# Kernel tuning notes

Measured on AMD Instinct MI355X. Metric: run time of the kernel, lower is better.

The kernel has to match this reference:

```python
import jax, jax.numpy as jnp
import numpy as np

B, T, D = 2, 4096, 768
H = 12
DK = D // H


def setup_inputs() -> dict:
    key = jax.random.key(0)
    k1, k2, k3 = jax.random.split(key, 3)
    x = jax.random.normal(k1, (B, T, D), dtype=jnp.float32)
    W_qkv = jax.random.normal(k2, (D, 3 * D), dtype=jnp.float32) * (1.0 / np.sqrt(D))
    b_qkv = jnp.zeros((3 * D,), dtype=jnp.float32)
    W_proj = jax.random.normal(k3, (D, D), dtype=jnp.float32) * (1.0 / np.sqrt(D))
    b_proj = jnp.zeros((D,), dtype=jnp.float32)
    return {"x": x, "W_qkv": W_qkv, "b_qkv": b_qkv, "W_proj": W_proj, "b_proj": b_proj}


def reference(x, W_qkv, b_qkv, W_proj, b_proj):
    b, t, c = x.shape
    qkv = x @ W_qkv + b_qkv                      # [B,T,3D]
    q, k, v = jnp.split(qkv, 3, axis=-1)
    q = q.reshape(b, t, H, DK)                   # [B,T,H,DK]
    k = k.reshape(b, t, H, DK)
    v = v.reshape(b, t, H, DK)
    scale = 1.0 / np.sqrt(DK)
    scores = jnp.einsum('bthd,bshd->bhts', q, k) * scale   # [B,H,T,T]
    causal = jnp.tril(jnp.ones((t, t), dtype=bool))
    scores = jnp.where(causal[None, None], scores, jnp.float32(-jnp.inf))
    probs = jax.nn.softmax(scores, axis=-1)      # dropout p=0.0 -> identity
    out = jnp.einsum('bhts,bshd->bthd', probs, v).reshape(b, t, c)
    return out @ W_proj + b_proj
```

## Files before the change

### kernel.cpp

```cpp
#include <hip/hip_runtime.h>
#include <hip/hip_bf16.h>
#include <cstdint>
#include <cstddef>


typedef __attribute__((ext_vector_type(8))) short bf16x8;
typedef __attribute__((ext_vector_type(4))) short bf16x4;
typedef __attribute__((ext_vector_type(4))) float f32x4;

#define MFMA16(a, b, c)   __builtin_amdgcn_mfma_f32_16x16x32_bf16((a), (b), (c), 0, 0, 0)
#define MFMA16K(a, b, c)  __builtin_amdgcn_mfma_f32_16x16x16bf16_1k((a), (b), (c), 0, 0, 0)

static constexpr int Bc = 2, Tc = 4096, Dc = 768, Hc = 12, DKc = 64;
static constexpr int BHc = Bc * Hc;
static constexpr int Mc = Bc * Tc;
static constexpr int Nqkv = 3 * Dc;
static constexpr int NQBLK = Tc / 128;
static constexpr unsigned int NITEMS = BHc * NQBLK;

__device__ __forceinline__ unsigned short f2bf(float f) {
    union { float f; unsigned int i; } c; c.f = f;
    unsigned int x = c.i;
    return (unsigned short)((x + 0x7fffu + ((x >> 16) & 1u)) >> 16);
}
__device__ __forceinline__ unsigned int pkbf(float a, float b) {
    __hip_bfloat162 h = __float22bfloat162_rn(make_float2(a, b));
    union { __hip_bfloat162 h; unsigned int u; } c; c.h = h;
    return c.u;
}
__device__ __forceinline__ void glds16(const unsigned short* g, unsigned short* l) {
    __builtin_amdgcn_global_load_lds(
        (const __attribute__((address_space(1))) unsigned int*)g,
        (__attribute__((address_space(3))) unsigned int*)l, 16, 0, 0);
}

__global__ __launch_bounds__(256)
void xconv_kernel(const float* __restrict__ X, unsigned short* __restrict__ Xb) {
    size_t i = ((size_t)blockIdx.x * 256 + threadIdx.x) * 8;
    float4 a = *(const float4*)(X + i);
    float4 b = *(const float4*)(X + i + 4);
    uint4 o;
    o.x = pkbf(a.x, a.y); o.y = pkbf(a.z, a.w);
    o.z = pkbf(b.x, b.y); o.w = pkbf(b.z, b.w);
    *(uint4*)(Xb + i) = o;
}

__global__ __launch_bounds__(256)
void wtrans_kernel(const float* __restrict__ W, unsigned short* __restrict__ WT,
                   int K, int N) {
    __shared__ __align__(16) unsigned short tile[64 * 72];
    const int k0 = blockIdx.x * 64;
    const int n0 = blockIdx.y * 64;
    const int tid = threadIdx.x;
#pragma unroll
    for (int it = 0; it < 4; ++it) {
        int s = tid + it * 256;
        int r = s >> 4, g = s & 15;
        float4 v = *(const float4*)(W + (size_t)(k0 + r) * N + n0 + g * 4);
        ushort4 u;
        u.x = f2bf(v.x); u.y = f2bf(v.y); u.z = f2bf(v.z); u.w = f2bf(v.w);
        *(ushort4*)(tile + r * 72 + g * 4) = u;
    }
    __syncthreads();
#pragma unroll
    for (int it = 0; it < 2; ++it) {
        int s = tid + it * 256;
        int n = s >> 3, g = s & 7;
        unsigned int p0 = (unsigned int)tile[(g * 8 + 0) * 72 + n] |
                          ((unsigned int)tile[(g * 8 + 1) * 72 + n] << 16);
        unsigned int p1 = (unsigned int)tile[(g * 8 + 2) * 72 + n] |
                          ((unsigned int)tile[(g * 8 + 3) * 72 + n] << 16);
        unsigned int p2 = (unsigned int)tile[(g * 8 + 4) * 72 + n] |
                          ((unsigned int)tile[(g * 8 + 5) * 72 + n] << 16);
        unsigned int p3 = (unsigned int)tile[(g * 8 + 6) * 72 + n] |
                          ((unsigned int)tile[(g * 8 + 7) * 72 + n] << 16);
        uint4 o; o.x = p0; o.y = p1; o.z = p2; o.w = p3;
        *(uint4*)(WT + (size_t)(n0 + n) * K + k0 + g * 8) = o;
    }
}

__global__ __launch_bounds__(256)
void qkv_gemm_kernel(const unsigned short* __restrict__ Xb,
                     const unsigned short* __restrict__ WT,
                     const float* __restrict__ bias,
                     unsigned short* __restrict__ Qb, unsigned short* __restrict__ Kb,
                     unsigned short* __restrict__ Vt) {
    __shared__ __align__(16) unsigned short As[128 * 64];
    __shared__ __align__(16) unsigned short Bs[128 * 64];
    const int tid = threadIdx.x;
    const int wave = tid >> 6, lane = tid & 63;
    const int quad = lane >> 4, l15 = lane & 15;
    const int wr = wave >> 1, wc = wave & 1;
    const int r0 = blockIdx.x * 128, c0 = blockIdx.y * 128;
    const int sw = l15 & 7;

    f32x4 acc[4][4];
#pragma unroll
    for (int i = 0; i < 4; ++i)
#pragma unroll
        for (int j = 0; j < 4; ++j) acc[i][j] = (f32x4){0.f, 0.f, 0.f, 0.f};

    for (int k0 = 0; k0 < Dc; k0 += 64) {
#pragma unroll
        for (int it = 0; it < 4; ++it) {
            int idx = it * 256 + tid;
            int r = idx >> 3, c = idx & 7;
            int cg = c ^ (r & 7);
            glds16(Xb + (size_t)(r0 + r) * Dc + k0 + cg * 8, As + idx * 8);
            glds16(WT + (size_t)(c0 + r) * Dc + k0 + cg * 8, Bs + idx * 8);
        }
        __syncthreads();
#pragma unroll
        for (int f = 0; f < 2; ++f) {
            bf16x8 af[4], bfr[4];
#pragma unroll
            for (int mt = 0; mt < 4; ++mt)
                af[mt] = *(const bf16x8*)(As + (wr * 64 + mt * 16 + l15) * 64 +
                                          (((f * 4 + quad) ^ sw) * 8));
#pragma unroll
            for (int nt = 0; nt < 4; ++nt)
                bfr[nt] = *(const bf16x8*)(Bs + (wc * 64 + nt * 16 + l15) * 64 +
                                           (((f * 4 + quad) ^ sw) * 8));
#pragma unroll
            for (int mt = 0; mt < 4; ++mt)
#pragma unroll
                for (int nt = 0; nt < 4; ++nt)
                    acc[mt][nt] = MFMA16(af[mt], bfr[nt], acc[mt][nt]);
        }
        __syncthreads();
    }

    const int part = c0 / Dc;
    const int cbase = c0 - part * Dc;
    const float scale = (part == 0) ? 0.125f * 1.4426950408889634f : 1.0f;
    float bv[4];
#pragma unroll
    for (int nt = 0; nt < 4; ++nt) bv[nt] = bias[c0 + wc * 64 + nt * 16 + l15];

    if (part < 2) {
        unsigned short* dstbuf = (part == 0) ? Qb : Kb;
#pragma unroll
        for (int mt = 0; mt < 4; ++mt)
#pragma unroll
            for (int reg = 0; reg < 4; ++reg) {
                int gr = r0 + wr * 64 + mt * 16 + quad * 4 + reg;
                int b = gr >> 12, t = gr & 4095;
#pragma unroll
                for (int nt = 0; nt < 4; ++nt) {
                    int cc = cbase + wc * 64 + nt * 16 + l15;
                    int h = cc >> 6, dk = cc & 63;
                    float v = (acc[mt][nt][reg] + bv[nt]) * scale;
                    dstbuf[((size_t)(b * Hc + h) * Tc + t) * DKc + dk] = f2bf(v);
                }
            }
    } else {
#pragma unroll
        for (int mt = 0; mt < 4; ++mt)
#pragma unroll
            for (int reg = 0; reg < 4; ++reg) {
                int gr = r0 + wr * 64 + mt * 16 + quad * 4 + reg;
                int b = gr >> 12, t = gr & 4095;
#pragma unroll
                for (int nt = 0; nt < 4; ++nt) {
                    int cc = cbase + wc * 64 + nt * 16 + l15;
                    int h = cc >> 6, dk = cc & 63;
                    float v = acc[mt][nt][reg] + bv[nt];
                    Vt[((size_t)(b * Hc + h) * DKc + dk) * Tc + t] = f2bf(v);
                }
            }
    }
}

__global__ __launch_bounds__(256)
void attn_kernel(const unsigned short* __restrict__ Qb,
                 const unsigned short* __restrict__ Kb,
                 const unsigned short* __restrict__ Vt,
                 unsigned short* __restrict__ attn,
                 unsigned int* __restrict__ counter) {
    __shared__ __align__(16) unsigned short Ks[64 * 64];
    __shared__ __align__(16) unsigned short Vs[64 * 64];
    __shared__ unsigned int s_w;
    const int tid = threadIdx.x;
    const int wave = tid >> 6, lane = tid & 63;
    const int quad = lane >> 4, l15 = lane & 15;
    const int sw = l15 & 7;

    for (;;) {
        if (tid == 0) s_w = atomicAdd(counter, 1u);
        __syncthreads();
        const unsigned int w = s_w;
        if (w >= NITEMS) break;
        const int bh = (int)(w % (unsigned)BHc);
        const int i0 = (NQBLK - 1 - (int)(w / (unsigned)BHc)) * 128;
        const unsigned short* Qp = Qb + (size_t)bh * Tc * DKc;
        const unsigned short* Kp = Kb + (size_t)bh * Tc * DKc;
        const unsigned short* Vp = Vt + (size_t)bh * DKc * Tc;

        bf16x8 qf[2][2];
#pragma unroll
        for (int qg = 0; qg < 2; ++qg)
#pragma unroll
            for (int f = 0; f < 2; ++f)
                qf[qg][f] = *(const bf16x8*)(Qp +
                    (size_t)(i0 + wave * 32 + qg * 16 + l15) * DKc + f * 32 + quad * 8);

        f32x4 lp[2] = {(f32x4){0.f,0.f,0.f,0.f}, (f32x4){0.f,0.f,0.f,0.f}};
        f32x4 o[2][4];
#pragma unroll
        for (int qg = 0; qg < 2; ++qg)
#pragma unroll
            for (int d = 0; d < 4; ++d) o[qg][d] = (f32x4){0.f, 0.f, 0.f, 0.f};

        const int jmax = (i0 >> 6) + 1;
        for (int jt = 0; jt <= jmax; ++jt) {
            const int j0 = jt * 64;
#pragma unroll
            for (int it = 0; it < 2; ++it) {
                int idx = it * 256 + tid;
                int r = idx >> 3, c = idx & 7;
                int cg = c ^ (r & 7);
                glds16(Kp + (size_t)(j0 + r) * DKc + cg * 8, Ks + idx * 8);
                glds16(Vp + (size_t)r * Tc + j0 + cg * 8, Vs + idx * 8);
            }
            __syncthreads();

            bf16x8 kf[2][4];
            bf16x4 vf[4][4];
#pragma unroll
            for (int f = 0; f < 2; ++f)
#pragma unroll
                for (int mt = 0; mt < 4; ++mt)
                    kf[f][mt] = *(const bf16x8*)(Ks + (mt * 16 + l15) * 64 +
                                                 (((f * 4 + quad) ^ sw) * 8));
#pragma unroll
            for (int d = 0; d < 4; ++d)
#pragma unroll
                for (int mt = 0; mt < 4; ++mt) {
                    int g8 = mt * 4 + quad;
                    vf[d][mt] = *(const bf16x4*)(Vs + (d * 16 + l15) * 64 +
                                                 (((g8 >> 1) ^ sw) * 8) + (g8 & 1) * 4);
                }
            __syncthreads();

            f32x4 sc[2][4];
#pragma unroll
            for (int qg = 0; qg < 2; ++qg)
#pragma unroll
                for (int mt = 0; mt < 4; ++mt) sc[qg][mt] = (f32x4){0.f, 0.f, 0.f, 0.f};
#pragma unroll
            for (int f = 0; f < 2; ++f)
#pragma unroll
                for (int mt = 0; mt < 4; ++mt) {
                    sc[0][mt] = MFMA16(kf[f][mt], qf[0][f], sc[0][mt]);
                    sc[1][mt] = MFMA16(kf[f][mt], qf[1][f], sc[1][mt]);
                }

            const int rel = j0 - i0;
            if (jt >= jmax - 1) {
#pragma unroll
                for (int qg = 0; qg < 2; ++qg) {
                    int qrow = wave * 32 + qg * 16 + l15;
#pragma unroll
                    for (int mt = 0; mt < 4; ++mt)
#pragma unroll
                        for (int reg = 0; reg < 4; ++reg)
                            if (rel + mt * 16 + quad * 4 + reg > qrow)
                                sc[qg][mt][reg] = -1e30f;
                }
            }

            union { uint2 u; bf16x4 v; } pb[2][4];
#pragma unroll
            for (int qg = 0; qg < 2; ++qg)
#pragma unroll
                for (int mt = 0; mt < 4; ++mt) {
#pragma unroll
                    for (int reg = 0; reg < 4; ++reg)
                        sc[qg][mt][reg] = __builtin_amdgcn_exp2f(sc[qg][mt][reg]);
                    lp[qg] += sc[qg][mt];
                    pb[qg][mt].u.x = pkbf(sc[qg][mt][0], sc[qg][mt][1]);
                    pb[qg][mt].u.y = pkbf(sc[qg][mt][2], sc[qg][mt][3]);
                }

#pragma unroll
            for (int mt = 0; mt < 4; ++mt)
#pragma unroll
                for (int d = 0; d < 4; ++d) {
                    o[0][d] = MFMA16K(vf[d][mt], pb[0][mt].v, o[0][d]);
                    o[1][d] = MFMA16K(vf[d][mt], pb[1][mt].v, o[1][d]);
                }
        }

        const int b = bh / Hc, h = bh % Hc;
#pragma unroll
        for (int qg = 0; qg < 2; ++qg) {
            float ls = lp[qg][0] + lp[qg][1] + lp[qg][2] + lp[qg][3];
            ls += __shfl_xor(ls, 16);
            ls += __shfl_xor(ls, 32);
            float li = 1.0f / ls;
            int t = i0 + wave * 32 + qg * 16 + l15;
            unsigned short* dst = attn + (size_t)(b * Tc + t) * Dc + h * 64;
#pragma unroll
            for (int d = 0; d < 4; ++d) {
                uint2 u;
                u.x = pkbf(o[qg][d][0] * li, o[qg][d][1] * li);
                u.y = pkbf(o[qg][d][2] * li, o[qg][d][3] * li);
                *(uint2*)(dst + d * 16 + quad * 4) = u;
            }
        }
    }
}

__global__ __launch_bounds__(256)
void proj_gemm_kernel(const unsigned short* __restrict__ A,
                      const unsigned short* __restrict__ WT,
                      const float* __restrict__ bias, float* __restrict__ out) {
    __shared__ __align__(16) unsigned short As[128 * 64];
    __shared__ __align__(16) unsigned short Bs[128 * 64];
    const int tid = threadIdx.x;
    const int wave = tid >> 6, lane = tid & 63;
    const int quad = lane >> 4, l15 = lane & 15;
    const int wr = wave >> 1, wc = wave & 1;
    const int r0 = blockIdx.x * 128, c0 = blockIdx.y * 128;
    const int sw = l15 & 7;

    f32x4 acc[4][4];
#pragma unroll
    for (int i = 0; i < 4; ++i)
#pragma unroll
        for (int j = 0; j < 4; ++j) acc[i][j] = (f32x4){0.f, 0.f, 0.f, 0.f};

    for (int k0 = 0; k0 < Dc; k0 += 64) {
#pragma unroll
        for (int it = 0; it < 4; ++it) {
            int idx = it * 256 + tid;
            int r = idx >> 3, c = idx & 7;
            int cg = c ^ (r & 7);
            glds16(A + (size_t)(r0 + r) * Dc + k0 + cg * 8, As + idx * 8);
            glds16(WT + (size_t)(c0 + r) * Dc + k0 + cg * 8, Bs + idx * 8);
        }
        __syncthreads();
#pragma unroll
        for (int f = 0; f < 2; ++f) {
            bf16x8 af[4], bfr[4];
#pragma unroll
            for (int mt = 0; mt < 4; ++mt)
                af[mt] = *(const bf16x8*)(As + (wr * 64 + mt * 16 + l15) * 64 +
                                          (((f * 4 + quad) ^ sw) * 8));
#pragma unroll
            for (int nt = 0; nt < 4; ++nt)
                bfr[nt] = *(const bf16x8*)(Bs + (wc * 64 + nt * 16 + l15) * 64 +
                                           (((f * 4 + quad) ^ sw) * 8));
#pragma unroll
            for (int mt = 0; mt < 4; ++mt)
#pragma unroll
                for (int nt = 0; nt < 4; ++nt)
                    acc[mt][nt] = MFMA16(af[mt], bfr[nt], acc[mt][nt]);
        }
        __syncthreads();
    }

    float bv[4];
#pragma unroll
    for (int nt = 0; nt < 4; ++nt) bv[nt] = bias[c0 + wc * 64 + nt * 16 + l15];
#pragma unroll
    for (int mt = 0; mt < 4; ++mt)
#pragma unroll
        for (int reg = 0; reg < 4; ++reg) {
            int gr = r0 + wr * 64 + mt * 16 + quad * 4 + reg;
#pragma unroll
            for (int nt = 0; nt < 4; ++nt) {
                int gc = c0 + wc * 64 + nt * 16 + l15;
                out[(size_t)gr * Dc + gc] = acc[mt][nt][reg] + bv[nt];
            }
        }
}

extern "C" void kernel_launch(void* const* d_in, const int* in_sizes, int n_in,
                              void* d_out, int out_size, void* d_ws, size_t ws_size,
                              hipStream_t stream) {
    const float* x      = (const float*)d_in[0];
    const float* W_qkv  = (const float*)d_in[1];
    const float* b_qkv  = (const float*)d_in[2];
    const float* W_proj = (const float*)d_in[3];
    const float* b_proj = (const float*)d_in[4];
    float* out = (float*)d_out;

    char* ws = (char*)d_ws;
    size_t off = 0;
    auto take = [&](size_t bytes) -> char* {
        char* p = ws + off;
        off += (bytes + 255) & ~(size_t)255;
        return p;
    };
    unsigned int*   cnt = (unsigned int*)take(256);
    unsigned short* WqT = (unsigned short*)take((size_t)Nqkv * Dc * 2);
    unsigned short* WpT = (unsigned short*)take((size_t)Dc * Dc * 2);
    unsigned short* Qb  = (unsigned short*)take((size_t)BHc * Tc * DKc * 2);
    unsigned short* Kb  = (unsigned short*)take((size_t)BHc * Tc * DKc * 2);
    unsigned short* Vt  = (unsigned short*)take((size_t)BHc * Tc * DKc * 2);
    unsigned short* Xb  = (unsigned short*)take((size_t)Mc * Dc * 2);
    unsigned short* An  = Xb;

    hipMemsetAsync(cnt, 0, sizeof(unsigned int), stream);
    xconv_kernel<<<dim3((Mc * Dc) / (256 * 8)), dim3(256), 0, stream>>>(x, Xb);
    wtrans_kernel<<<dim3(Dc / 64, Nqkv / 64), dim3(256), 0, stream>>>(W_qkv, WqT, Dc, Nqkv);
    wtrans_kernel<<<dim3(Dc / 64, Dc / 64), dim3(256), 0, stream>>>(W_proj, WpT, Dc, Dc);
    qkv_gemm_kernel<<<dim3(Mc / 128, Nqkv / 128), dim3(256), 0, stream>>>(Xb, WqT, b_qkv, Qb, Kb, Vt);
    attn_kernel<<<dim3(NITEMS), dim3(256), 0, stream>>>(Qb, Kb, Vt, An, cnt);
    proj_gemm_kernel<<<dim3(Mc / 128, Dc / 128), dim3(256), 0, stream>>>(An, WpT, b_proj, out);
}
```

Baseline: 258.2 us.

## Merge weight transposes, use MFMA row sums in attention, narrow proj tiles

Merges the two weight-transpose launches into one grid that picks W_qkv or W_proj by block row, saving a launch. In attention, the softmax denominator is now accumulated with an MFMA against a ones vector instead of vector adds plus cross-lane shuffles. The second barrier only waits on LDS reads (lgkmcnt) rather than doing a full __syncthreads, and the score MFMAs start from zero instead of clearing registers first. The projection GEMM uses 128x64 tiles to double its block count for better CU occupancy, at the cost of reloading the A tile more often.

```diff
diff --git a/kernel.cpp b/kernel.cpp
--- a/kernel.cpp
+++ b/kernel.cpp
@@ -46,11 +46,16 @@
 }
 
 __global__ __launch_bounds__(256)
-void wtrans_kernel(const float* __restrict__ W, unsigned short* __restrict__ WT,
-                   int K, int N) {
+void wtrans_kernel(const float* __restrict__ Wq, const float* __restrict__ Wp,
+                   unsigned short* __restrict__ WqT, unsigned short* __restrict__ WpT) {
     __shared__ __align__(16) unsigned short tile[64 * 72];
     const int k0 = blockIdx.x * 64;
-    const int n0 = blockIdx.y * 64;
+    const int yb = blockIdx.y;
+    const float* W;
+    unsigned short* WT;
+    int N, n0;
+    if (yb < 36) { W = Wq; WT = WqT; N = Nqkv; n0 = yb * 64; }
+    else         { W = Wp; WT = WpT; N = Dc;   n0 = (yb - 36) * 64; }
     const int tid = threadIdx.x;
 #pragma unroll
     for (int it = 0; it < 4; ++it) {
@@ -75,7 +80,7 @@
         unsigned int p3 = (unsigned int)tile[(g * 8 + 6) * 72 + n] |
                           ((unsigned int)tile[(g * 8 + 7) * 72 + n] << 16);
         uint4 o; o.x = p0; o.y = p1; o.z = p2; o.w = p3;
-        *(uint4*)(WT + (size_t)(n0 + n) * K + k0 + g * 8) = o;
+        *(uint4*)(WT + (size_t)(n0 + n) * Dc + k0 + g * 8) = o;
     }
 }
 
@@ -184,6 +189,9 @@
     const int wave = tid >> 6, lane = tid & 63;
     const int quad = lane >> 4, l15 = lane & 15;
     const int sw = l15 & 7;
+    const f32x4 czero = (f32x4){0.f, 0.f, 0.f, 0.f};
+    const bf16x4 ones = (bf16x4){(short)0x3F80, (short)0x3F80,
+                                 (short)0x3F80, (short)0x3F80};
 
     for (;;) {
         if (tid == 0) s_w = atomicAdd(counter, 1u);
@@ -204,7 +212,7 @@
                 qf[qg][f] = *(const bf16x8*)(Qp +
                     (size_t)(i0 + wave * 32 + qg * 16 + l15) * DKc + f * 32 + quad * 8);
 
-        f32x4 lp[2] = {(f32x4){0.f,0.f,0.f,0.f}, (f32x4){0.f,0.f,0.f,0.f}};
+        f32x4 lsum[2] = {czero, czero};
         f32x4 o[2][4];
 #pragma unroll
         for (int qg = 0; qg < 2; ++qg)
@@ -240,20 +248,20 @@
                     vf[d][mt] = *(const bf16x4*)(Vs + (d * 16 + l15) * 64 +
                                                  (((g8 >> 1) ^ sw) * 8) + (g8 & 1) * 4);
                 }
-            __syncthreads();
+            asm volatile("s_waitcnt lgkmcnt(0)" ::: "memory");
+            __builtin_amdgcn_s_barrier();
 
             f32x4 sc[2][4];
 #pragma unroll
-            for (int qg = 0; qg < 2; ++qg)
-#pragma unroll
-                for (int mt = 0; mt < 4; ++mt) sc[qg][mt] = (f32x4){0.f, 0.f, 0.f, 0.f};
-#pragma unroll
-            for (int f = 0; f < 2; ++f)
-#pragma unroll
-                for (int mt = 0; mt < 4; ++mt) {
-                    sc[0][mt] = MFMA16(kf[f][mt], qf[0][f], sc[0][mt]);
-                    sc[1][mt] = MFMA16(kf[f][mt], qf[1][f], sc[1][mt]);
-                }
+            for (int mt = 0; mt < 4; ++mt) {
+                sc[0][mt] = MFMA16(kf[0][mt], qf[0][0], czero);
+                sc[1][mt] = MFMA16(kf[0][mt], qf[1][0], czero);
+            }
+#pragma unroll
+            for (int mt = 0; mt < 4; ++mt) {
+                sc[0][mt] = MFMA16(kf[1][mt], qf[0][1], sc[0][mt]);
+                sc[1][mt] = MFMA16(kf[1][mt], qf[1][1], sc[1][mt]);
+            }
 
             const int rel = j0 - i0;
             if (jt >= jmax - 1) {
@@ -277,27 +285,26 @@
 #pragma unroll
                     for (int reg = 0; reg < 4; ++reg)
                         sc[qg][mt][reg] = __builtin_amdgcn_exp2f(sc[qg][mt][reg]);
-                    lp[qg] += sc[qg][mt];
                     pb[qg][mt].u.x = pkbf(sc[qg][mt][0], sc[qg][mt][1]);
                     pb[qg][mt].u.y = pkbf(sc[qg][mt][2], sc[qg][mt][3]);
                 }
 
 #pragma unroll
-            for (int mt = 0; mt < 4; ++mt)
+            for (int mt = 0; mt < 4; ++mt) {
+                lsum[0] = MFMA16K(ones, pb[0][mt].v, lsum[0]);
+                lsum[1] = MFMA16K(ones, pb[1][mt].v, lsum[1]);
 #pragma unroll
                 for (int d = 0; d < 4; ++d) {
                     o[0][d] = MFMA16K(vf[d][mt], pb[0][mt].v, o[0][d]);
                     o[1][d] = MFMA16K(vf[d][mt], pb[1][mt].v, o[1][d]);
                 }
+            }
         }
 
         const int b = bh / Hc, h = bh % Hc;
 #pragma unroll
         for (int qg = 0; qg < 2; ++qg) {
-            float ls = lp[qg][0] + lp[qg][1] + lp[qg][2] + lp[qg][3];
-            ls += __shfl_xor(ls, 16);
-            ls += __shfl_xor(ls, 32);
-            float li = 1.0f / ls;
+            float li = 1.0f / lsum[qg][0];
             int t = i0 + wave * 32 + qg * 16 + l15;
             unsigned short* dst = attn + (size_t)(b * Tc + t) * Dc + h * 64;
 #pragma unroll
@@ -316,61 +323,65 @@
                       const unsigned short* __restrict__ WT,
                       const float* __restrict__ bias, float* __restrict__ out) {
     __shared__ __align__(16) unsigned short As[128 * 64];
-    __shared__ __align__(16) unsigned short Bs[128 * 64];
+    __shared__ __align__(16) unsigned short Bs[64 * 64];
     const int tid = threadIdx.x;
     const int wave = tid >> 6, lane = tid & 63;
     const int quad = lane >> 4, l15 = lane & 15;
     const int wr = wave >> 1, wc = wave & 1;
-    const int r0 = blockIdx.x * 128, c0 = blockIdx.y * 128;
+    const int r0 = blockIdx.x * 128, c0 = blockIdx.y * 64;
     const int sw = l15 & 7;
 
-    f32x4 acc[4][4];
+    f32x4 acc[4][2];
 #pragma unroll
     for (int i = 0; i < 4; ++i)
 #pragma unroll
-        for (int j = 0; j < 4; ++j) acc[i][j] = (f32x4){0.f, 0.f, 0.f, 0.f};
+        for (int j = 0; j < 2; ++j) acc[i][j] = (f32x4){0.f, 0.f, 0.f, 0.f};
 
     for (int k0 = 0; k0 < Dc; k0 += 64) {
 #pragma unroll
         for (int it = 0; it < 4; ++it) {
             int idx = it * 256 + tid;
             int r = idx >> 3, c = idx & 7;
-            int cg = c ^ (r & 7);
-            glds16(A + (size_t)(r0 + r) * Dc + k0 + cg * 8, As + idx * 8);
-            glds16(WT + (size_t)(c0 + r) * Dc + k0 + cg * 8, Bs + idx * 8);
+            glds16(A + (size_t)(r0 + r) * Dc + k0 + ((c ^ (r & 7)) * 8), As + idx * 8);
+        }
+#pragma unroll
+        for (int it = 0; it < 2; ++it) {
+            int idx = it * 256 + tid;
+            int r = idx >> 3, c = idx & 7;
+            glds16(WT + (size_t)(c0 + r) * Dc + k0 + ((c ^ (r & 7)) * 8), Bs + idx * 8);
         }
         __syncthreads();
 #pragma unroll
         for (int f = 0; f < 2; ++f) {
-            bf16x8 af[4], bfr[4];
+            bf16x8 af[4], bfr[2];
 #pragma unroll
             for (int mt = 0; mt < 4; ++mt)
                 af[mt] = *(const bf16x8*)(As + (wr * 64 + mt * 16 + l15) * 64 +
                                           (((f * 4 + quad) ^ sw) * 8));
 #pragma unroll
-            for (int nt = 0; nt < 4; ++nt)
-                bfr[nt] = *(const bf16x8*)(Bs + (wc * 64 + nt * 16 + l15) * 64 +
+            for (int nt = 0; nt < 2; ++nt)
+                bfr[nt] = *(const bf16x8*)(Bs + (wc * 32 + nt * 16 + l15) * 64 +
                                            (((f * 4 + quad) ^ sw) * 8));
 #pragma unroll
             for (int mt = 0; mt < 4; ++mt)
 #pragma unroll
-                for (int nt = 0; nt < 4; ++nt)
+                for (int nt = 0; nt < 2; ++nt)
                     acc[mt][nt] = MFMA16(af[mt], bfr[nt], acc[mt][nt]);
         }
         __syncthreads();
     }
 
-    float bv[4];
-#pragma unroll
-    for (int nt = 0; nt < 4; ++nt) bv[nt] = bias[c0 + wc * 64 + nt * 16 + l15];
+    float bv[2];
+#pragma unroll
+    for (int nt = 0; nt < 2; ++nt) bv[nt] = bias[c0 + wc * 32 + nt * 16 + l15];
 #pragma unroll
     for (int mt = 0; mt < 4; ++mt)
 #pragma unroll
         for (int reg = 0; reg < 4; ++reg) {
             int gr = r0 + wr * 64 + mt * 16 + quad * 4 + reg;
 #pragma unroll
-            for (int nt = 0; nt < 4; ++nt) {
-                int gc = c0 + wc * 64 + nt * 16 + l15;
+            for (int nt = 0; nt < 2; ++nt) {
+                int gc = c0 + wc * 32 + nt * 16 + l15;
                 out[(size_t)gr * Dc + gc] = acc[mt][nt][reg] + bv[nt];
             }
         }
@@ -404,9 +415,8 @@
 
     hipMemsetAsync(cnt, 0, sizeof(unsigned int), stream);
     xconv_kernel<<<dim3((Mc * Dc) / (256 * 8)), dim3(256), 0, stream>>>(x, Xb);
-    wtrans_kernel<<<dim3(Dc / 64, Nqkv / 64), dim3(256), 0, stream>>>(W_qkv, WqT, Dc, Nqkv);
-    wtrans_kernel<<<dim3(Dc / 64, Dc / 64), dim3(256), 0, stream>>>(W_proj, WpT, Dc, Dc);
+    wtrans_kernel<<<dim3(Dc / 64, (Nqkv + Dc) / 64), dim3(256), 0, stream>>>(W_qkv, W_proj, WqT, WpT);
     qkv_gemm_kernel<<<dim3(Mc / 128, Nqkv / 128), dim3(256), 0, stream>>>(Xb, WqT, b_qkv, Qb, Kb, Vt);
     attn_kernel<<<dim3(NITEMS), dim3(256), 0, stream>>>(Qb, Kb, Vt, An, cnt);
-    proj_gemm_kernel<<<dim3(Mc / 128, Dc / 128), dim3(256), 0, stream>>>(An, WpT, b_proj, out);
-}
+    proj_gemm_kernel<<<dim3(Mc / 128, Dc / 64), dim3(256), 0, stream>>>(An, WpT, b_proj, out);
+}
```

Result: no change. 253.6 us (-1.8%).
